# Kernel optimization log

Hardware: AMD Instinct MI355X
Metric: run time of the kernel (lower is better)

Reference implementation:

```python
import jax, jax.numpy as jnp
import numpy as np

N_NODES = 50000
N_EDGES = 800000
IN_CH = 64
HID = 128
LAST_HID = 256


def setup_inputs() -> dict:
    key = jax.random.key(0)
    ks = jax.random.split(key, 12)
    x = jax.random.normal(ks[0], (N_NODES, IN_CH), dtype=jnp.float32)
    edge_index = jax.random.randint(ks[1], (2, N_EDGES), 0, N_NODES, dtype=jnp.int64)
    s = lambda fan_in: 1.0 / np.sqrt(fan_in)
    return {
        "x": x,
        "edge_index": edge_index,
        # SAGEConv1: lin_l (aggregated neighbors, with bias), lin_r (root, no bias)
        "W1l": jax.random.normal(ks[2], (HID, IN_CH), dtype=jnp.float32) * s(IN_CH),
        "b1l": jnp.zeros((HID,), dtype=jnp.float32),
        "W1r": jax.random.normal(ks[3], (HID, IN_CH), dtype=jnp.float32) * s(IN_CH),
        # SAGEConv2 -> 1 channel
        "W2l": jax.random.normal(ks[4], (1, HID), dtype=jnp.float32) * s(HID),
        "b2l": jnp.zeros((1,), dtype=jnp.float32),
        "W2r": jax.random.normal(ks[5], (1, HID), dtype=jnp.float32) * s(HID),
        # fc1 (LazyLinear bound to N_NODES input features) and fc2
        "fc1_W": jax.random.normal(ks[6], (LAST_HID, N_NODES), dtype=jnp.float32) * s(N_NODES),
        "fc1_b": jnp.zeros((LAST_HID,), dtype=jnp.float32),
        "fc2_W": jax.random.normal(ks[7], (1, LAST_HID), dtype=jnp.float32) * s(LAST_HID),
        "fc2_b": jnp.zeros((1,), dtype=jnp.float32),
    }


def _sage_conv(h, src, dst, Wl, bl, Wr, n_nodes):
    # PyG SAGEConv (mean aggr): out = lin_l(mean_{j in N(i)} x_j) + lin_r(x_i)
    msgs = h[src]  # [E, F] gather of source node features
    summed = jax.ops.segment_sum(msgs, dst, num_segments=n_nodes)  # [N, F]
    deg = jax.ops.segment_sum(jnp.ones((src.shape[0],), h.dtype), dst, num_segments=n_nodes)
    agg = summed / jnp.maximum(deg, 1.0)[:, None]
    return agg @ Wl.T + bl + h @ Wr.T


def reference(x, edge_index, W1l, b1l, W1r, W2l, b2l, W2r, fc1_W, fc1_b, fc2_W, fc2_b):
    n = x.shape[0]
    src, dst = edge_index[0], edge_index[1]
    h = jax.nn.relu(_sage_conv(x, src, dst, W1l, b1l, W1r, n))   # [N, HID]
    h = jax.nn.relu(_sage_conv(h, src, dst, W2l, b2l, W2r, n))   # [N, 1]
    v = h[:, 0]                                                   # [N]
    z = fc1_W @ v + fc1_b                                         # [LAST_HID]
    pred = fc2_W @ z + fc2_b                                      # [1]
    return pred[0]  # scalar (torch.squeeze)
```

## Files before the change

### kernel.cpp

```cpp
#include <hip/hip_runtime.h>

#define N_NODESC 50000
#define N_EDGESC 800000
#define MAXDEG 64

typedef short bf16x8 __attribute__((ext_vector_type(8)));
typedef float f32x4  __attribute__((ext_vector_type(4)));

__device__ inline unsigned short f2bf(float f) {
    unsigned u = __float_as_uint(f);
    unsigned r = u + 0x7FFFu + ((u >> 16) & 1u);
    return (unsigned short)(r >> 16);
}
__device__ inline float bf2f(unsigned short h) {
    return __uint_as_float(((unsigned)h) << 16);
}

__global__ void k0_init(int* __restrict__ deg, float* __restrict__ z) {
    int i = blockIdx.x * 256 + threadIdx.x;
    if (i < N_NODESC) deg[i] = 0;
    if (i < 256) z[i] = 0.0f;
}

__global__ void kW_pack(const float* __restrict__ W1l, const float* __restrict__ W1r,
                        short* __restrict__ pkhi, short* __restrict__ pklo) {
    int ks = blockIdx.x;
    int t  = threadIdx.x;
    int o  = t & 127;
    int h  = t >> 7;
    const float* src = (ks < 2) ? (W1r + o * 64 + ks * 32)
                                : (W1l + o * 64 + (ks - 2) * 32);
    #pragma unroll
    for (int qi = 0; qi < 2; qi++) {
        int q = 2 * h + qi;
        float4 a = *(const float4*)(src + q * 8);
        float4 b = *(const float4*)(src + q * 8 + 4);
        float v[8] = {a.x, a.y, a.z, a.w, b.x, b.y, b.z, b.w};
        bf16x8 hv, lv;
        #pragma unroll
        for (int j = 0; j < 8; j++) {
            unsigned short hh = f2bf(v[j]);
            hv[j] = (short)hh;
            lv[j] = (short)f2bf(v[j] - bf2f(hh));
        }
        int idx = ((ks * 4 + q) * 128 + o) * 8;
        *(bf16x8*)&pkhi[idx] = hv;
        *(bf16x8*)&pklo[idx] = lv;
    }
}

#define K1_BLOCKS 2048
#define K1_EPB (N_EDGESC / (K1_BLOCKS / 8))
__global__ void k1_bucket(const int* __restrict__ ei, int* __restrict__ deg,
                          int* __restrict__ bucket) {
    int g   = blockIdx.x & 7;
    int idx = blockIdx.x >> 3;
    int lo = g * (N_NODESC / 8), hi = lo + (N_NODESC / 8);
    int e0 = idx * K1_EPB;
    for (int i = threadIdx.x; i < K1_EPB; i += 256) {
        int e = e0 + i;
        int dst = ei[N_EDGESC + e];
        int src = ei[e];
        if (dst >= lo && dst < hi) {
            int slot = atomicAdd(&deg[dst], 1);
            if (slot < MAXDEG) bucket[dst * MAXDEG + slot] = src;
        }
    }
}

__global__ void k2_agg(const float* __restrict__ x, const int* __restrict__ deg,
                       const int* __restrict__ bucket, float* __restrict__ agg) {
    int lane = threadIdx.x & 63;
    int node = blockIdx.x * 4 + (threadIdx.x >> 6);
    int g  = lane >> 4;
    int c4 = lane & 15;
    int d = deg[node];
    int c = min(d, MAXDEG);
    int bidx = bucket[node * MAXDEG + lane];
    float4 acc = make_float4(0.f, 0.f, 0.f, 0.f);
    for (int k = 0; k < c; k += 8) {
        int i0 = k + g, i1 = k + 4 + g;
        int b0 = __shfl(bidx, i0);
        int b1 = __shfl(bidx, i1);
        if (i0 < c) {
            float4 v = ((const float4*)(x + b0 * 64))[c4];
            acc.x += v.x; acc.y += v.y; acc.z += v.z; acc.w += v.w;
        }
        if (i1 < c) {
            float4 v = ((const float4*)(x + b1 * 64))[c4];
            acc.x += v.x; acc.y += v.y; acc.z += v.z; acc.w += v.w;
        }
    }
    #pragma unroll
    for (int m = 16; m <= 32; m <<= 1) {
        acc.x += __shfl_xor(acc.x, m);
        acc.y += __shfl_xor(acc.y, m);
        acc.z += __shfl_xor(acc.z, m);
        acc.w += __shfl_xor(acc.w, m);
    }
    if (g == 0) {
        float inv = 1.0f / (float)max(d, 1);
        ((float4*)(agg + node * 64))[c4] =
            make_float4(acc.x * inv, acc.y * inv, acc.z * inv, acc.w * inv);
    }
}

#define K3S 144

__launch_bounds__(256, 3)
__global__ void k3_mm_mfma(const float* __restrict__ x, const float* __restrict__ agg,
                           const short* __restrict__ pkhi, const short* __restrict__ pklo,
                           const float* __restrict__ b1l,
                           const float* __restrict__ W2l, const float* __restrict__ W2r,
                           float* __restrict__ s_out, float* __restrict__ t_out) {
    __shared__ __align__(16) short sAhi[64 * K3S];
    __shared__ __align__(16) short sAlo[64 * K3S];
    __shared__ float sSp[4][64], sTp[4][64];

    int tid = threadIdx.x;
    int lane = tid & 63;
    int wave = tid >> 6;
    int col = lane & 15;
    int quad = lane >> 4;
    int node0 = blockIdx.x * 64;

    float4 sv0[4], sv1[4];
    #pragma unroll
    for (int i = 0; i < 4; i++) {
        int c = tid + 256 * i;
        int n = c >> 4, kc = c & 15;
        int node = node0 + n;
        if (node < N_NODESC) {
            const float* src = (kc < 8) ? (x + node * 64 + kc * 8)
                                        : (agg + node * 64 + (kc - 8) * 8);
            sv0[i] = *(const float4*)src;
            sv1[i] = *(const float4*)(src + 4);
        } else {
            sv0[i] = make_float4(0.f, 0.f, 0.f, 0.f);
            sv1[i] = make_float4(0.f, 0.f, 0.f, 0.f);
        }
    }

    int o_base = wave * 32;
    bf16x8 bhi[2][4], blo[2][4];
    float bias_r[2], w2l_r[2], w2r_r[2];
    #pragma unroll
    for (int oc = 0; oc < 2; oc++) {
        int o = o_base + oc * 16 + col;
        bias_r[oc] = b1l[o]; w2l_r[oc] = W2l[o]; w2r_r[oc] = W2r[o];
        #pragma unroll
        for (int ks = 0; ks < 4; ks++) {
            int idx = ((ks * 4 + quad) * 128 + o) * 8;
            bhi[oc][ks] = *(const bf16x8*)&pkhi[idx];
            blo[oc][ks] = *(const bf16x8*)&pklo[idx];
        }
    }

    #pragma unroll
    for (int i = 0; i < 4; i++) {
        int c = tid + 256 * i;
        int n = c >> 4, kc = c & 15;
        float v[8] = {sv0[i].x, sv0[i].y, sv0[i].z, sv0[i].w,
                      sv1[i].x, sv1[i].y, sv1[i].z, sv1[i].w};
        bf16x8 hv, lv;
        #pragma unroll
        for (int j = 0; j < 8; j++) {
            unsigned short h = f2bf(v[j]);
            hv[j] = (short)h;
            lv[j] = (short)f2bf(v[j] - bf2f(h));
        }
        *(bf16x8*)&sAhi[n * K3S + kc * 8] = hv;
        *(bf16x8*)&sAlo[n * K3S + kc * 8] = lv;
    }
    __syncthreads();

    f32x4 acc[4][2];
    #pragma unroll
    for (int nt = 0; nt < 4; nt++)
        #pragma unroll
        for (int oc = 0; oc < 2; oc++) acc[nt][oc] = (f32x4)0.f;

    #pragma unroll
    for (int ks = 0; ks < 4; ks++) {
        #pragma unroll
        for (int nt = 0; nt < 4; nt++) {
            int off = (nt * 16 + col) * K3S + ks * 32 + quad * 8;
            bf16x8 ah = *(const bf16x8*)&sAhi[off];
            bf16x8 al = *(const bf16x8*)&sAlo[off];
            #pragma unroll
            for (int oc = 0; oc < 2; oc++) {
                acc[nt][oc] = __builtin_amdgcn_mfma_f32_16x16x32_bf16(ah, bhi[oc][ks], acc[nt][oc], 0, 0, 0);
                acc[nt][oc] = __builtin_amdgcn_mfma_f32_16x16x32_bf16(al, bhi[oc][ks], acc[nt][oc], 0, 0, 0);
                acc[nt][oc] = __builtin_amdgcn_mfma_f32_16x16x32_bf16(ah, blo[oc][ks], acc[nt][oc], 0, 0, 0);
            }
        }
    }

    #pragma unroll
    for (int nt = 0; nt < 4; nt++) {
        float sp[4] = {0.f, 0.f, 0.f, 0.f};
        float tp[4] = {0.f, 0.f, 0.f, 0.f};
        #pragma unroll
        for (int oc = 0; oc < 2; oc++)
            #pragma unroll
            for (int reg = 0; reg < 4; reg++) {
                float h = fmaxf(acc[nt][oc][reg] + bias_r[oc], 0.f);
                sp[reg] += h * w2l_r[oc];
                tp[reg] += h * w2r_r[oc];
            }
        #pragma unroll
        for (int reg = 0; reg < 4; reg++) {
            #pragma unroll
            for (int m = 1; m <= 8; m <<= 1) {
                sp[reg] += __shfl_xor(sp[reg], m);
                tp[reg] += __shfl_xor(tp[reg], m);
            }
        }
        if (col == 0) {
            int nn = nt * 16 + quad * 4;
            #pragma unroll
            for (int reg = 0; reg < 4; reg++) {
                sSp[wave][nn + reg] = sp[reg];
                sTp[wave][nn + reg] = tp[reg];
            }
        }
    }
    __syncthreads();
    if (tid < 64) {
        int node = node0 + tid;
        if (node < N_NODESC) {
            s_out[node] = sSp[0][tid] + sSp[1][tid] + sSp[2][tid] + sSp[3][tid];
            t_out[node] = sTp[0][tid] + sTp[1][tid] + sTp[2][tid] + sTp[3][tid];
        }
    }
}

__global__ void k4_layer2(const float* __restrict__ s, const float* __restrict__ t,
                          const int* __restrict__ deg, const int* __restrict__ bucket,
                          const float* __restrict__ b2l, float* __restrict__ v) {
    int tid = threadIdx.x;
    int lane = tid & 15;
    int node = blockIdx.x * 16 + (tid >> 4);
    int d = deg[node];
    int c = min(d, MAXDEG);
    float sum = 0.f;
    for (int k = lane; k < c; k += 16) sum += s[bucket[node * MAXDEG + k]];
    sum += __shfl_xor(sum, 1);
    sum += __shfl_xor(sum, 2);
    sum += __shfl_xor(sum, 4);
    sum += __shfl_xor(sum, 8);
    if (lane == 0) {
        float h = sum / (float)max(d, 1) + b2l[0] + t[node];
        v[node] = fmaxf(h, 0.f);
    }
}

__global__ void k5_fc1(const float* __restrict__ fc1W, const float* __restrict__ v,
                       float* __restrict__ z) {
    int row = blockIdx.x >> 2;
    int part = blockIdx.x & 3;
    const float4* W4 = (const float4*)(fc1W + row * 50000 + part * 12500);
    const float4* v4 = (const float4*)(v + part * 12500);
    float sum = 0.f;
    for (int i = threadIdx.x; i < 3125; i += 256) {
        float4 w = W4[i], a = v4[i];
        sum += w.x * a.x + w.y * a.y + w.z * a.z + w.w * a.w;
    }
    #pragma unroll
    for (int m = 1; m < 64; m <<= 1) sum += __shfl_xor(sum, m);
    __shared__ float red[4];
    if ((threadIdx.x & 63) == 0) red[threadIdx.x >> 6] = sum;
    __syncthreads();
    if (threadIdx.x == 0) atomicAdd(&z[row], red[0] + red[1] + red[2] + red[3]);
}

__global__ void k6_head(const float* __restrict__ z, const float* __restrict__ fc1b,
                        const float* __restrict__ fc2W, const float* __restrict__ fc2b,
                        float* __restrict__ out) {
    int t = threadIdx.x;
    float val = (z[t] + fc1b[t]) * fc2W[t];
    #pragma unroll
    for (int m = 1; m < 64; m <<= 1) val += __shfl_xor(val, m);
    __shared__ float red[4];
    if ((t & 63) == 0) red[t >> 6] = val;
    __syncthreads();
    if (t == 0) out[0] = red[0] + red[1] + red[2] + red[3] + fc2b[0];
}

extern "C" void kernel_launch(void* const* d_in, const int* in_sizes, int n_in,
                              void* d_out, int out_size, void* d_ws, size_t ws_size,
                              hipStream_t stream) {
    const float* x    = (const float*)d_in[0];
    const int*   ei   = (const int*)d_in[1];
    const float* W1l  = (const float*)d_in[2];
    const float* b1l  = (const float*)d_in[3];
    const float* W1r  = (const float*)d_in[4];
    const float* W2l  = (const float*)d_in[5];
    const float* b2l  = (const float*)d_in[6];
    const float* W2r  = (const float*)d_in[7];
    const float* fc1W = (const float*)d_in[8];
    const float* fc1b = (const float*)d_in[9];
    const float* fc2W = (const float*)d_in[10];
    const float* fc2b = (const float*)d_in[11];
    float* out = (float*)d_out;

    char* ws = (char*)d_ws;
    int*   deg    = (int*)  (ws + 0);
    float* z      = (float*)(ws + 200192);
    int*   bucket = (int*)  (ws + 201216);
    float* agg    = (float*)(ws + 13001216);
    float* s      = (float*)(ws + 25801216);
    float* t      = (float*)(ws + 26001216);
    float* v      = (float*)(ws + 26201216);
    short* pkhi   = (short*)(ws + 26401280);
    short* pklo   = (short*)(ws + 26434048);

    k0_init   <<<196,   256, 0, stream>>>(deg, z);
    kW_pack   <<<4,     256, 0, stream>>>(W1l, W1r, pkhi, pklo);
    k1_bucket <<<K1_BLOCKS, 256, 0, stream>>>(ei, deg, bucket);
    k2_agg    <<<12500, 256, 0, stream>>>(x, deg, bucket, agg);
    k3_mm_mfma<<<782,  256, 0, stream>>>(x, agg, pkhi, pklo, b1l, W2l, W2r, s, t);
    k4_layer2 <<<3125,  256, 0, stream>>>(s, t, deg, bucket, b2l, v);
    k5_fc1    <<<1024,  256, 0, stream>>>(fc1W, v, z);
    k6_head   <<<1,     256, 0, stream>>>(z, fc1b, fc2W, fc2b, out);
}
```

Baseline: 210.2 us.

## Fuse neighbor aggregation into MFMA layer-1 kernel and merge init/pack and head kernels

The layer-1 mean aggregation is now computed inside the MFMA kernel, with each wave gathering 16 nodes and writing split bf16 hi/lo values straight into shared memory. This removes the separate agg kernel and the 12.8 MB agg buffer write and read. The init and weight-pack kernels are merged into one launch. The final head reduction runs in the last fc1 block, found through an atomic counter, which removes another launch. The trade-off is that the fused kernel has only 782 blocks, each looping over 16 nodes per wave, so there is less parallelism to hide gather latency than the old 12500-block aggregation kernel had.

```diff
diff --git a/kernel.cpp b/kernel.cpp
--- a/kernel.cpp
+++ b/kernel.cpp
@@ -5,6 +5,7 @@
 #define MAXDEG 64
 
 typedef short bf16x8 __attribute__((ext_vector_type(8)));
+typedef short short4v __attribute__((ext_vector_type(4)));
 typedef float f32x4  __attribute__((ext_vector_type(4)));
 
 __device__ inline unsigned short f2bf(float f) {
@@ -16,36 +17,38 @@
     return __uint_as_float(((unsigned)h) << 16);
 }
 
-__global__ void k0_init(int* __restrict__ deg, float* __restrict__ z) {
+__global__ void kW0_init_pack(const float* __restrict__ W1l, const float* __restrict__ W1r,
+                              short* __restrict__ pkhi, short* __restrict__ pklo,
+                              int* __restrict__ deg, float* __restrict__ z,
+                              int* __restrict__ ctr) {
     int i = blockIdx.x * 256 + threadIdx.x;
     if (i < N_NODESC) deg[i] = 0;
     if (i < 256) z[i] = 0.0f;
-}
-
-__global__ void kW_pack(const float* __restrict__ W1l, const float* __restrict__ W1r,
-                        short* __restrict__ pkhi, short* __restrict__ pklo) {
-    int ks = blockIdx.x;
-    int t  = threadIdx.x;
-    int o  = t & 127;
-    int h  = t >> 7;
-    const float* src = (ks < 2) ? (W1r + o * 64 + ks * 32)
-                                : (W1l + o * 64 + (ks - 2) * 32);
-    #pragma unroll
-    for (int qi = 0; qi < 2; qi++) {
-        int q = 2 * h + qi;
-        float4 a = *(const float4*)(src + q * 8);
-        float4 b = *(const float4*)(src + q * 8 + 4);
-        float v[8] = {a.x, a.y, a.z, a.w, b.x, b.y, b.z, b.w};
-        bf16x8 hv, lv;
-        #pragma unroll
-        for (int j = 0; j < 8; j++) {
-            unsigned short hh = f2bf(v[j]);
-            hv[j] = (short)hh;
-            lv[j] = (short)f2bf(v[j] - bf2f(hh));
-        }
-        int idx = ((ks * 4 + q) * 128 + o) * 8;
-        *(bf16x8*)&pkhi[idx] = hv;
-        *(bf16x8*)&pklo[idx] = lv;
+    if (i == 0) ctr[0] = 0;
+    if (blockIdx.x < 4) {
+        int ks = blockIdx.x;
+        int t  = threadIdx.x;
+        int o  = t & 127;
+        int h  = t >> 7;
+        const float* src = (ks < 2) ? (W1r + o * 64 + ks * 32)
+                                    : (W1l + o * 64 + (ks - 2) * 32);
+        #pragma unroll
+        for (int qi = 0; qi < 2; qi++) {
+            int q = 2 * h + qi;
+            float4 a = *(const float4*)(src + q * 8);
+            float4 b = *(const float4*)(src + q * 8 + 4);
+            float v[8] = {a.x, a.y, a.z, a.w, b.x, b.y, b.z, b.w};
+            bf16x8 hv, lv;
+            #pragma unroll
+            for (int j = 0; j < 8; j++) {
+                unsigned short hh = f2bf(v[j]);
+                hv[j] = (short)hh;
+                lv[j] = (short)f2bf(v[j] - bf2f(hh));
+            }
+            int idx = ((ks * 4 + q) * 128 + o) * 8;
+            *(bf16x8*)&pkhi[idx] = hv;
+            *(bf16x8*)&pklo[idx] = lv;
+        }
     }
 }
 
@@ -68,51 +71,15 @@
     }
 }
 
-__global__ void k2_agg(const float* __restrict__ x, const int* __restrict__ deg,
-                       const int* __restrict__ bucket, float* __restrict__ agg) {
-    int lane = threadIdx.x & 63;
-    int node = blockIdx.x * 4 + (threadIdx.x >> 6);
-    int g  = lane >> 4;
-    int c4 = lane & 15;
-    int d = deg[node];
-    int c = min(d, MAXDEG);
-    int bidx = bucket[node * MAXDEG + lane];
-    float4 acc = make_float4(0.f, 0.f, 0.f, 0.f);
-    for (int k = 0; k < c; k += 8) {
-        int i0 = k + g, i1 = k + 4 + g;
-        int b0 = __shfl(bidx, i0);
-        int b1 = __shfl(bidx, i1);
-        if (i0 < c) {
-            float4 v = ((const float4*)(x + b0 * 64))[c4];
-            acc.x += v.x; acc.y += v.y; acc.z += v.z; acc.w += v.w;
-        }
-        if (i1 < c) {
-            float4 v = ((const float4*)(x + b1 * 64))[c4];
-            acc.x += v.x; acc.y += v.y; acc.z += v.z; acc.w += v.w;
-        }
-    }
-    #pragma unroll
-    for (int m = 16; m <= 32; m <<= 1) {
-        acc.x += __shfl_xor(acc.x, m);
-        acc.y += __shfl_xor(acc.y, m);
-        acc.z += __shfl_xor(acc.z, m);
-        acc.w += __shfl_xor(acc.w, m);
-    }
-    if (g == 0) {
-        float inv = 1.0f / (float)max(d, 1);
-        ((float4*)(agg + node * 64))[c4] =
-            make_float4(acc.x * inv, acc.y * inv, acc.z * inv, acc.w * inv);
-    }
-}
-
 #define K3S 144
 
 __launch_bounds__(256, 3)
-__global__ void k3_mm_mfma(const float* __restrict__ x, const float* __restrict__ agg,
-                           const short* __restrict__ pkhi, const short* __restrict__ pklo,
-                           const float* __restrict__ b1l,
-                           const float* __restrict__ W2l, const float* __restrict__ W2r,
-                           float* __restrict__ s_out, float* __restrict__ t_out) {
+__global__ void k3_fused(const float* __restrict__ x,
+                         const int* __restrict__ deg, const int* __restrict__ bucket,
+                         const short* __restrict__ pkhi, const short* __restrict__ pklo,
+                         const float* __restrict__ b1l,
+                         const float* __restrict__ W2l, const float* __restrict__ W2r,
+                         float* __restrict__ s_out, float* __restrict__ t_out) {
     __shared__ __align__(16) short sAhi[64 * K3S];
     __shared__ __align__(16) short sAlo[64 * K3S];
     __shared__ float sSp[4][64], sTp[4][64];
@@ -124,15 +91,14 @@
     int quad = lane >> 4;
     int node0 = blockIdx.x * 64;
 
-    float4 sv0[4], sv1[4];
-    #pragma unroll
-    for (int i = 0; i < 4; i++) {
+    float4 sv0[2], sv1[2];
+    #pragma unroll
+    for (int i = 0; i < 2; i++) {
         int c = tid + 256 * i;
-        int n = c >> 4, kc = c & 15;
+        int n = c >> 3, kc = c & 7;
         int node = node0 + n;
         if (node < N_NODESC) {
-            const float* src = (kc < 8) ? (x + node * 64 + kc * 8)
-                                        : (agg + node * 64 + (kc - 8) * 8);
+            const float* src = x + node * 64 + kc * 8;
             sv0[i] = *(const float4*)src;
             sv1[i] = *(const float4*)(src + 4);
         } else {
@@ -157,9 +123,9 @@
     }
 
     #pragma unroll
-    for (int i = 0; i < 4; i++) {
+    for (int i = 0; i < 2; i++) {
         int c = tid + 256 * i;
-        int n = c >> 4, kc = c & 15;
+        int n = c >> 3, kc = c & 7;
         float v[8] = {sv0[i].x, sv0[i].y, sv0[i].z, sv0[i].w,
                       sv1[i].x, sv1[i].y, sv1[i].z, sv1[i].w};
         bf16x8 hv, lv;
@@ -171,6 +137,67 @@
         }
         *(bf16x8*)&sAhi[n * K3S + kc * 8] = hv;
         *(bf16x8*)&sAlo[n * K3S + kc * 8] = lv;
+    }
+
+    {
+        int node_p = node0 + wave * 16;
+        int d_cur = 0, b_cur = 0;
+        if (node_p < N_NODESC) {
+            d_cur = deg[node_p];
+            b_cur = bucket[node_p * MAXDEG + lane];
+        }
+        for (int nl = 0; nl < 16; nl++) {
+            int node_n = node0 + wave * 16 + nl + 1;
+            int d_nxt = 0, b_nxt = 0;
+            if (nl < 15 && node_n < N_NODESC) {
+                d_nxt = deg[node_n];
+                b_nxt = bucket[node_n * MAXDEG + lane];
+            }
+            int nloc = wave * 16 + nl;
+            int node = node0 + nloc;
+            if (node < N_NODESC) {
+                int cdeg = min(d_cur, MAXDEG);
+                float4 acc = make_float4(0.f, 0.f, 0.f, 0.f);
+                for (int k = 0; k < cdeg; k += 8) {
+                    int i0 = k + quad, i1 = k + 4 + quad;
+                    int b0 = __shfl(b_cur, i0);
+                    int b1 = __shfl(b_cur, i1);
+                    if (i0 < cdeg) {
+                        float4 v = ((const float4*)(x + b0 * 64))[col];
+                        acc.x += v.x; acc.y += v.y; acc.z += v.z; acc.w += v.w;
+                    }
+                    if (i1 < cdeg) {
+                        float4 v = ((const float4*)(x + b1 * 64))[col];
+                        acc.x += v.x; acc.y += v.y; acc.z += v.z; acc.w += v.w;
+                    }
+                }
+                #pragma unroll
+                for (int m = 16; m <= 32; m <<= 1) {
+                    acc.x += __shfl_xor(acc.x, m);
+                    acc.y += __shfl_xor(acc.y, m);
+                    acc.z += __shfl_xor(acc.z, m);
+                    acc.w += __shfl_xor(acc.w, m);
+                }
+                if (quad == 0) {
+                    float inv = 1.0f / (float)max(d_cur, 1);
+                    float vv[4] = {acc.x * inv, acc.y * inv, acc.z * inv, acc.w * inv};
+                    short4v hv, lv;
+                    #pragma unroll
+                    for (int j = 0; j < 4; j++) {
+                        unsigned short h = f2bf(vv[j]);
+                        hv[j] = (short)h;
+                        lv[j] = (short)f2bf(vv[j] - bf2f(h));
+                    }
+                    *(short4v*)&sAhi[nloc * K3S + 64 + col * 4] = hv;
+                    *(short4v*)&sAlo[nloc * K3S + 64 + col * 4] = lv;
+                }
+            } else if (quad == 0) {
+                short4v zz = (short4v)0;
+                *(short4v*)&sAhi[nloc * K3S + 64 + col * 4] = zz;
+                *(short4v*)&sAlo[nloc * K3S + 64 + col * 4] = zz;
+            }
+            d_cur = d_nxt; b_cur = b_nxt;
+        }
     }
     __syncthreads();
 
@@ -256,7 +283,9 @@
 }
 
 __global__ void k5_fc1(const float* __restrict__ fc1W, const float* __restrict__ v,
-                       float* __restrict__ z) {
+                       float* __restrict__ z, int* __restrict__ ctr,
+                       const float* __restrict__ fc1b, const float* __restrict__ fc2W,
+                       const float* __restrict__ fc2b, float* __restrict__ out) {
     int row = blockIdx.x >> 2;
     int part = blockIdx.x & 3;
     const float4* W4 = (const float4*)(fc1W + row * 50000 + part * 12500);
@@ -272,19 +301,22 @@
     if ((threadIdx.x & 63) == 0) red[threadIdx.x >> 6] = sum;
     __syncthreads();
     if (threadIdx.x == 0) atomicAdd(&z[row], red[0] + red[1] + red[2] + red[3]);
-}
-
-__global__ void k6_head(const float* __restrict__ z, const float* __restrict__ fc1b,
-                        const float* __restrict__ fc2W, const float* __restrict__ fc2b,
-                        float* __restrict__ out) {
-    int t = threadIdx.x;
-    float val = (z[t] + fc1b[t]) * fc2W[t];
-    #pragma unroll
-    for (int m = 1; m < 64; m <<= 1) val += __shfl_xor(val, m);
-    __shared__ float red[4];
-    if ((t & 63) == 0) red[t >> 6] = val;
+
+    __threadfence();
+    __shared__ int lastv;
+    if (threadIdx.x == 0) lastv = atomicAdd(ctr, 1);
     __syncthreads();
-    if (t == 0) out[0] = red[0] + red[1] + red[2] + red[3] + fc2b[0];
+    if (lastv == 1023) {
+        int t = threadIdx.x;
+        float zv = __hip_atomic_load(&z[t], __ATOMIC_RELAXED, __HIP_MEMORY_SCOPE_AGENT);
+        float val = (zv + fc1b[t]) * fc2W[t];
+        #pragma unroll
+        for (int m = 1; m < 64; m <<= 1) val += __shfl_xor(val, m);
+        __shared__ float red2[4];
+        if ((t & 63) == 0) red2[t >> 6] = val;
+        __syncthreads();
+        if (t == 0) out[0] = red2[0] + red2[1] + red2[2] + red2[3] + fc2b[0];
+    }
 }
 
 extern "C" void kernel_launch(void* const* d_in, const int* in_sizes, int n_in,
@@ -307,20 +339,17 @@
     char* ws = (char*)d_ws;
     int*   deg    = (int*)  (ws + 0);
     float* z      = (float*)(ws + 200192);
-    int*   bucket = (int*)  (ws + 201216);
-    float* agg    = (float*)(ws + 13001216);
-    float* s      = (float*)(ws + 25801216);
-    float* t      = (float*)(ws + 26001216);
-    float* v      = (float*)(ws + 26201216);
-    short* pkhi   = (short*)(ws + 26401280);
-    short* pklo   = (short*)(ws + 26434048);
-
-    k0_init   <<<196,   256, 0, stream>>>(deg, z);
-    kW_pack   <<<4,     256, 0, stream>>>(W1l, W1r, pkhi, pklo);
-    k1_bucket <<<K1_BLOCKS, 256, 0, stream>>>(ei, deg, bucket);
-    k2_agg    <<<12500, 256, 0, stream>>>(x, deg, bucket, agg);
-    k3_mm_mfma<<<782,  256, 0, stream>>>(x, agg, pkhi, pklo, b1l, W2l, W2r, s, t);
-    k4_layer2 <<<3125,  256, 0, stream>>>(s, t, deg, bucket, b2l, v);
-    k5_fc1    <<<1024,  256, 0, stream>>>(fc1W, v, z);
-    k6_head   <<<1,     256, 0, stream>>>(z, fc1b, fc2W, fc2b, out);
-}
+    int*   ctr    = (int*)  (ws + 201216);
+    int*   bucket = (int*)  (ws + 201728);
+    float* s      = (float*)(ws + 13001728);
+    float* t      = (float*)(ws + 13201728);
+    float* v      = (float*)(ws + 13401728);
+    short* pkhi   = (short*)(ws + 13601792);
+    short* pklo   = (short*)(ws + 13634560);
+
+    kW0_init_pack<<<196,  256, 0, stream>>>(W1l, W1r, pkhi, pklo, deg, z, ctr);
+    k1_bucket    <<<K1_BLOCKS, 256, 0, stream>>>(ei, deg, bucket);
+    k3_fused     <<<782,  256, 0, stream>>>(x, deg, bucket, pkhi, pklo, b1l, W2l, W2r, s, t);
+    k4_layer2    <<<3125, 256, 0, stream>>>(s, t, deg, bucket, b2l, v);
+    k5_fc1       <<<1024, 256, 0, stream>>>(fc1W, v, z, ctr, fc1b, fc2W, fc2b, out);
+}
```

Result: slower. 297.5 us (+41.5%).
